# Kernel tuning notes

Measured on AMD Instinct MI355X. Metric: run time of the kernel, lower is better.

## Reference

```python
import jax, jax.numpy as jnp
import numpy as np

B, S, HID, H = 4, 2048, 768, 12
HD = HID // H  # head dim = 64
EPS = 1e-12


def _linear(x, w, b):
    # x: [B,S,HID], w: [HID,OUT] (already transposed to in x out), b: [OUT]
    return jnp.einsum('bsi,io->bso', x, w) + b


def _heads(x):
    # [B,S,HID] -> [B,H,S,HD]
    return x.reshape(B, S, H, HD).transpose(0, 2, 1, 3)


def _layernorm(x, g, b):
    mu = jnp.mean(x, axis=-1, keepdims=True)
    var = jnp.mean(jnp.square(x - mu), axis=-1, keepdims=True)
    return (x - mu) * jax.lax.rsqrt(var + EPS) * g + b


def _attend(q, k, v, mask):
    # q:[B,H,Sq,HD] k,v:[B,H,Sk,HD] mask:[B,1,1,Sk] additive
    scores = jnp.einsum('bhqd,bhkd->bhqk', q, k) / np.float32(np.sqrt(HD)) + mask
    probs = jax.nn.softmax(scores, axis=-1)  # dropout is identity in eval
    ctx = jnp.einsum('bhqk,bhkd->bhqd', probs, v)
    return ctx.transpose(0, 2, 1, 3).reshape(B, S, HID)


def setup_inputs() -> dict:
    key = jax.random.key(0)
    ks = jax.random.split(key, 20)
    std = 0.02
    mkw = lambda k: (jax.random.normal(k, (HID, HID), jnp.float32) * std)
    inp = {
        'input_tensor1': jax.random.normal(ks[0], (B, S, HID), jnp.float32),
        'attention_mask1': jnp.zeros((B, 1, 1, S), jnp.float32),
        'input_tensor2': jax.random.normal(ks[1], (B, S, HID), jnp.float32),
        'attention_mask2': jnp.zeros((B, 1, 1, S), jnp.float32),
        'q1_w': mkw(ks[2]), 'q1_b': jnp.zeros(HID),
        'k1_w': mkw(ks[3]), 'k1_b': jnp.zeros(HID),
        'v1_w': mkw(ks[4]), 'v1_b': jnp.zeros(HID),
        'q2_w': mkw(ks[5]), 'q2_b': jnp.zeros(HID),
        'k2_w': mkw(ks[6]), 'k2_b': jnp.zeros(HID),
        'v2_w': mkw(ks[7]), 'v2_b': jnp.zeros(HID),
        'd1_w': mkw(ks[8]), 'd1_b': jnp.zeros(HID),
        'd2_w': mkw(ks[9]), 'd2_b': jnp.zeros(HID),
        'ln1_g': jnp.ones(HID), 'ln1_b': jnp.zeros(HID),
        'ln2_g': jnp.ones(HID), 'ln2_b': jnp.zeros(HID),
    }
    return inp


def reference(input_tensor1, attention_mask1, input_tensor2, attention_mask2,
              q1_w, q1_b, k1_w, k1_b, v1_w, v1_b,
              q2_w, q2_b, k2_w, k2_b, v2_w, v2_b,
              d1_w, d1_b, d2_w, d2_b, ln1_g, ln1_b, ln2_g, ln2_b):
    q1 = _heads(_linear(input_tensor1, q1_w, q1_b))
    k1 = _heads(_linear(input_tensor1, k1_w, k1_b))
    v1 = _heads(_linear(input_tensor1, v1_w, v1_b))
    q2 = _heads(_linear(input_tensor2, q2_w, q2_b))
    k2 = _heads(_linear(input_tensor2, k2_w, k2_b))
    v2 = _heads(_linear(input_tensor2, v2_w, v2_b))
    # stream1 context: queries from stream2 attend keys/values of stream1
    ctx1 = _attend(q2, k1, v1, attention_mask1)
    # stream2 context: queries from stream1 attend keys/values of stream2
    ctx2 = _attend(q1, k2, v2, attention_mask2)
    h1 = _layernorm(_linear(ctx1, d1_w, d1_b) + input_tensor1, ln1_g, ln1_b)
    h2 = _layernorm(_linear(ctx2, d2_w, d2_b) + input_tensor2, ln2_g, ln2_b)
    return (h1, h2)
```

## Files before the change

### kernel.cpp

```cpp
#include <hip/hip_runtime.h>
#include <hip/hip_bf16.h>

#define BB   4
#define SS   2048
#define HID_ 768
#define NH   12
#define HD_  64
#define MR   8192
#define XELEMS 6291456

typedef __attribute__((ext_vector_type(8))) short short8;
typedef __attribute__((ext_vector_type(4))) float floatx4;

__device__ __forceinline__ unsigned short f2bf(float f) {
  union { float f; unsigned int u; } x; x.f = f;
  unsigned int r = x.u + 0x7fffu + ((x.u >> 16) & 1u);
  return (unsigned short)(r >> 16);
}

__device__ __forceinline__ unsigned short f2bf_fast(float f) {
  return (unsigned short)((__builtin_bit_cast(unsigned int, f) + 0x8000u) >> 16);
}

template <int CTRL>
__device__ __forceinline__ float dpp_ror(float x) {
  return __builtin_bit_cast(float, __builtin_amdgcn_update_dpp(
      0, __builtin_bit_cast(int, x), CTRL, 0xF, 0xF, true));
}
__device__ __forceinline__ float rowsum16(float x) {
  x += dpp_ror<0x128>(x);
  x += dpp_ror<0x124>(x);
  x += dpp_ror<0x122>(x);
  x += dpp_ror<0x121>(x);
  return x;
}

__device__ __forceinline__ void gload_lds16(const unsigned short* g, unsigned short* l) {
  __builtin_amdgcn_global_load_lds(
      (const __attribute__((address_space(1))) unsigned int*)g,
      (__attribute__((address_space(3))) unsigned int*)l, 16, 0, 0);
}

__global__ __launch_bounds__(256)
void cast_kernel(const float* __restrict__ src, unsigned short* __restrict__ dst, int n) {
  int i = (blockIdx.x * 256 + threadIdx.x) * 4;
  if (i < n) {
    float4 v = *(const float4*)(src + i);
    ushort4 o;
    o.x = f2bf(v.x); o.y = f2bf(v.y); o.z = f2bf(v.z); o.w = f2bf(v.w);
    *(ushort4*)(dst + i) = o;
  }
}

struct WArgs { const float* src[8]; unsigned short* dst[8]; };

__global__ __launch_bounds__(256)
void wcast_kernel(WArgs args) {
  __shared__ float tile[32][33];
  const int w = blockIdx.z;
  const float* __restrict__ src = args.src[w];
  unsigned short* __restrict__ dst = args.dst[w];
  const int n0 = blockIdx.x * 32, k0 = blockIdx.y * 32;
  const int tx = threadIdx.x & 31, ty = threadIdx.x >> 5;
  #pragma unroll
  for (int i = 0; i < 4; ++i)
    tile[ty + 8 * i][tx] = src[(size_t)(k0 + ty + 8 * i) * HID_ + n0 + tx];
  __syncthreads();
  #pragma unroll
  for (int i = 0; i < 4; ++i)
    dst[(size_t)(n0 + ty + 8 * i) * HID_ + k0 + tx] = f2bf(tile[tx][ty + 8 * i]);
}

struct GemmArgs {
  const unsigned short* A[6];
  const unsigned short* Bt[6];
  const float* bias[6];
  const float* resid[6];
  unsigned short* outb[6];
  float* outf[6];
  int tmode[6];
};

template <int MODE>
__global__ __launch_bounds__(256)
void gemm_kernel(GemmArgs args) {
  const int z = blockIdx.z;
  const unsigned short* __restrict__ A  = args.A[z];
  const unsigned short* __restrict__ Bt = args.Bt[z];
  const int m0 = blockIdx.x * 128;
  const int n0 = blockIdx.y * 128;

  __shared__ __align__(16) unsigned short a_sh[128 * 32];
  __shared__ __align__(16) unsigned short b_sh[128 * 32];

  const int tid  = threadIdx.x;
  const int lane = tid & 63;
  const int wave = tid >> 6;
  const int wm = (wave & 1) * 64;
  const int wn = (wave >> 1) * 64;
  const int l15 = lane & 15;
  const int ko  = lane >> 4;

  floatx4 acc[4][4];
  #pragma unroll
  for (int mt = 0; mt < 4; ++mt)
    #pragma unroll
    for (int nt = 0; nt < 4; ++nt) {
      floatx4 zz = {0.f, 0.f, 0.f, 0.f};
      acc[mt][nt] = zz;
    }

  const int ch0 = wave * 2;
  size_t aoff[2], boff[2];
  unsigned short *adst[2], *bdst[2];
  #pragma unroll
  for (int j = 0; j < 2; ++j) {
    const int ch = ch0 + j;
    const int row = ch * 16 + (lane >> 2);
    const int col = (lane & 3) * 8;
    aoff[j] = (size_t)(m0 + row) * 768 + col;
    boff[j] = (size_t)(n0 + row) * 768 + col;
    adst[j] = a_sh + ch * 512 + lane * 8;
    bdst[j] = b_sh + ch * 512 + lane * 8;
  }

  for (int k0 = 0; k0 < 768; k0 += 32) {
    #pragma unroll
    for (int j = 0; j < 2; ++j) {
      gload_lds16(A  + aoff[j] + k0, adst[j]);
      gload_lds16(Bt + boff[j] + k0, bdst[j]);
    }
    __syncthreads();
    short8 af[4], bfr[4];
    #pragma unroll
    for (int t = 0; t < 4; ++t) {
      af[t]  = *(const short8*)(a_sh + (wm + t * 16 + l15) * 32 + ko * 8);
      bfr[t] = *(const short8*)(b_sh + (wn + t * 16 + l15) * 32 + ko * 8);
    }
    #pragma unroll
    for (int mt = 0; mt < 4; ++mt)
      #pragma unroll
      for (int nt = 0; nt < 4; ++nt)
        acc[mt][nt] = __builtin_amdgcn_mfma_f32_16x16x32_bf16(af[mt], bfr[nt], acc[mt][nt], 0, 0, 0);
    __syncthreads();
  }

  if (MODE == 0) {
    const float* __restrict__ bias = args.bias[z];
    unsigned short* __restrict__ out = args.outb[z];
    if (args.tmode[z] == 0) {
      #pragma unroll
      for (int mt = 0; mt < 4; ++mt) {
        const int gm = m0 + wm + mt * 16 + ko * 4;
        #pragma unroll
        for (int nt = 0; nt < 4; ++nt) {
          const int gn = n0 + wn + nt * 16 + l15;
          const float bv = bias[gn];
          #pragma unroll
          for (int r = 0; r < 4; ++r)
            out[(size_t)(gm + r) * 768 + gn] = f2bf(acc[mt][nt][r] + bv);
        }
      }
    } else {
      #pragma unroll
      for (int mt = 0; mt < 4; ++mt) {
        const int gm = m0 + wm + mt * 16 + ko * 4;
        const int bb_ = gm >> 11;
        const int s   = gm & 2047;
        #pragma unroll
        for (int nt = 0; nt < 4; ++nt) {
          const int gn = n0 + wn + nt * 16 + l15;
          const float bv = bias[gn];
          const int h = gn >> 6, d = gn & 63;
          ushort4 o4;
          o4.x = f2bf(acc[mt][nt][0] + bv);
          o4.y = f2bf(acc[mt][nt][1] + bv);
          o4.z = f2bf(acc[mt][nt][2] + bv);
          o4.w = f2bf(acc[mt][nt][3] + bv);
          *(ushort4*)(out + ((size_t)((bb_ * 12 + h) * 64 + d)) * 2048 + s) = o4;
        }
      }
    }
  } else {
    const float* __restrict__ bias  = args.bias[z];
    const float* __restrict__ resid = args.resid[z];
    float* __restrict__ out = args.outf[z];
    #pragma unroll
    for (int mt = 0; mt < 4; ++mt) {
      const int gm = m0 + wm + mt * 16 + ko * 4;
      #pragma unroll
      for (int nt = 0; nt < 4; ++nt) {
        const int gn = n0 + wn + nt * 16 + l15;
        const float bv = bias[gn];
        #pragma unroll
        for (int r = 0; r < 4; ++r)
          out[(size_t)(gm + r) * 768 + gn] = acc[mt][nt][r] + bv + resid[(size_t)(gm + r) * 768 + gn];
      }
    }
  }
}

struct AttnArgs {
  const unsigned short* q[2];
  const unsigned short* k[2];
  const unsigned short* vt[2];
  const float* mask[2];
  unsigned short* ctx[2];
};

__global__ __launch_bounds__(256)
void attn_kernel(AttnArgs args) {
  const int z = blockIdx.z;
  const int b = z >> 1, w = z & 1;
  const int h = blockIdx.y;
  const int q0 = blockIdx.x * 64;

  const unsigned short* __restrict__ Q  = args.q[1 - w];
  const unsigned short* __restrict__ K  = args.k[w];
  const unsigned short* __restrict__ Vt = args.vt[w] + ((size_t)(b * 12 + h)) * 64 * 2048;
  const float* __restrict__ mask = args.mask[w] + (size_t)b * SS;
  unsigned short* __restrict__ O = args.ctx[w];

  __shared__ __align__(16) unsigned short k_sh[64 * 72];
  __shared__ __align__(16) unsigned short vT_sh[64 * 72];
  __shared__ __align__(16) unsigned short p_sh[4][16 * 72];

  const int tid  = threadIdx.x;
  const int lane = tid & 63;
  const int wave = tid >> 6;
  const int l15 = lane & 15;
  const int lq  = lane >> 4;

  const size_t qrow = (size_t)(b * SS + q0 + wave * 16 + l15) * 768 + h * 64;
  short8 qf[2];
  qf[0] = *(const short8*)(Q + qrow + lq * 8);
  qf[1] = *(const short8*)(Q + qrow + 32 + lq * 8);

  floatx4 oacc[4];
  #pragma unroll
  for (int nt = 0; nt < 4; ++nt) { floatx4 zz = {0.f,0.f,0.f,0.f}; oacc[nt] = zz; }
  float l_run[4] = {0.f, 0.f, 0.f, 0.f};

  const float SCL2 = 0.125f * 1.4426950408889634f;

  for (int kt = 0; kt < SS; kt += 64) {
    #pragma unroll
    for (int i = 0; i < 2; ++i) {
      const int c = tid * 2 + i;
      const int row = c >> 3;
      const int cb  = (c & 7) * 8;
      uint4 kv4 = *(const uint4*)(K + (size_t)(b * SS + kt + row) * 768 + h * 64 + cb);
      *(uint4*)(k_sh + row * 72 + cb) = kv4;
      uint4 vv4 = *(const uint4*)(Vt + (size_t)row * 2048 + kt + cb);
      *(uint4*)(vT_sh + row * 72 + cb) = vv4;
    }
    __syncthreads();

    floatx4 sacc[4];
    #pragma unroll
    for (int nt = 0; nt < 4; ++nt) {
      floatx4 zz = {0.f,0.f,0.f,0.f};
      sacc[nt] = zz;
      #pragma unroll
      for (int ks = 0; ks < 2; ++ks) {
        short8 bfr = *(const short8*)(k_sh + (nt * 16 + l15) * 72 + ks * 32 + lq * 8);
        sacc[nt] = __builtin_amdgcn_mfma_f32_16x16x32_bf16(qf[ks], bfr, sacc[nt], 0, 0, 0);
      }
    }

    float p[4][4], lad[4] = {0.f, 0.f, 0.f, 0.f};
    #pragma unroll
    for (int nt = 0; nt < 4; ++nt) {
      const float mk2 = mask[kt + nt * 16 + l15] * 1.4426950408889634f;
      #pragma unroll
      for (int r = 0; r < 4; ++r) {
        p[nt][r] = __builtin_amdgcn_exp2f(sacc[nt][r] * SCL2 + mk2);
        lad[r] += p[nt][r];
      }
    }
    #pragma unroll
    for (int r = 0; r < 4; ++r) l_run[r] += rowsum16(lad[r]);

    unsigned short* pw = p_sh[wave];
    #pragma unroll
    for (int nt = 0; nt < 4; ++nt)
      #pragma unroll
      for (int r = 0; r < 4; ++r)
        pw[(lq * 4 + r) * 72 + nt * 16 + l15] = f2bf_fast(p[nt][r]);

    #pragma unroll
    for (int nt = 0; nt < 4; ++nt) {
      #pragma unroll
      for (int ks = 0; ks < 2; ++ks) {
        short8 pf = *(const short8*)(pw + l15 * 72 + ks * 32 + lq * 8);
        short8 vf = *(const short8*)(vT_sh + (nt * 16 + l15) * 72 + ks * 32 + lq * 8);
        oacc[nt] = __builtin_amdgcn_mfma_f32_16x16x32_bf16(pf, vf, oacc[nt], 0, 0, 0);
      }
    }
    __syncthreads();
  }

  float inv[4];
  #pragma unroll
  for (int r = 0; r < 4; ++r) inv[r] = 1.f / l_run[r];
  #pragma unroll
  for (int nt = 0; nt < 4; ++nt) {
    #pragma unroll
    for (int r = 0; r < 4; ++r) {
      const int gq = q0 + wave * 16 + lq * 4 + r;
      const int gd = h * 64 + nt * 16 + l15;
      O[(size_t)(b * SS + gq) * 768 + gd] = f2bf(oacc[nt][r] * inv[r]);
    }
  }
}

__global__ __launch_bounds__(256)
void ln_kernel(const float* __restrict__ src, const float* __restrict__ g,
               const float* __restrict__ bta, float* __restrict__ out) {
  const int row = blockIdx.x;
  const int tid = threadIdx.x;
  const float* x = src + (size_t)row * 768;
  const float v0 = x[tid], v1 = x[tid + 256], v2 = x[tid + 512];
  float sum = v0 + v1 + v2;
  float sq  = v0 * v0 + v1 * v1 + v2 * v2;
  #pragma unroll
  for (int d = 1; d < 64; d <<= 1) {
    sum += __shfl_xor(sum, d, 64);
    sq  += __shfl_xor(sq, d, 64);
  }
  __shared__ float ssum[4], ssq[4];
  const int wave = tid >> 6, lane = tid & 63;
  if (lane == 0) { ssum[wave] = sum; ssq[wave] = sq; }
  __syncthreads();
  sum = ssum[0] + ssum[1] + ssum[2] + ssum[3];
  sq  = ssq[0] + ssq[1] + ssq[2] + ssq[3];
  const float mean = sum * (1.f / 768.f);
  const float var  = sq * (1.f / 768.f) - mean * mean;
  const float rs   = rsqrtf(var + 1e-12f);
  float* o = out + (size_t)row * 768;
  o[tid]       = (v0 - mean) * rs * g[tid]       + bta[tid];
  o[tid + 256] = (v1 - mean) * rs * g[tid + 256] + bta[tid + 256];
  o[tid + 512] = (v2 - mean) * rs * g[tid + 512] + bta[tid + 512];
}

extern "C" void kernel_launch(void* const* d_in, const int* in_sizes, int n_in,
                              void* d_out, int out_size, void* d_ws, size_t ws_size,
                              hipStream_t stream) {
  const float* x1    = (const float*)d_in[0];
  const float* mask1 = (const float*)d_in[1];
  const float* x2    = (const float*)d_in[2];
  const float* mask2 = (const float*)d_in[3];

  char* ws = (char*)d_ws;
  const size_t SZ_X = (size_t)MR * HID_ * 2;
  const size_t SZ_W = (size_t)HID_ * HID_ * 2;

  unsigned short* xb0 = (unsigned short*)(ws);
  unsigned short* xb1 = (unsigned short*)(ws + SZ_X);
  unsigned short* wtb[8];
  for (int i = 0; i < 8; ++i) wtb[i] = (unsigned short*)(ws + 2 * SZ_X + i * SZ_W);
  char* qbase = ws + 2 * SZ_X + 8 * SZ_W;
  unsigned short* qkvb[6];
  for (int i = 0; i < 6; ++i) qkvb[i] = (unsigned short*)(qbase + i * SZ_X);
  unsigned short* ctxb[2];
  ctxb[0] = (unsigned short*)(qbase + 6 * SZ_X);
  ctxb[1] = (unsigned short*)(qbase + 7 * SZ_X);
  float* projb[2];
  projb[0] = (float*)(qbase);
  projb[1] = (float*)(qbase + 2 * SZ_X);

  cast_kernel<<<XELEMS / 1024, 256, 0, stream>>>(x1, xb0, XELEMS);
  cast_kernel<<<XELEMS / 1024, 256, 0, stream>>>(x2, xb1, XELEMS);

  WArgs wa;
  for (int z = 0; z < 8; ++z) { wa.src[z] = (const float*)d_in[4 + 2 * z]; wa.dst[z] = wtb[z]; }
  wcast_kernel<<<dim3(24, 24, 8), 256, 0, stream>>>(wa);

  GemmArgs ga = {};
  for (int z = 0; z < 6; ++z) {
    ga.A[z]    = (z < 3) ? xb0 : xb1;
    ga.Bt[z]   = wtb[z];
    ga.bias[z] = (const float*)d_in[5 + 2 * z];
    ga.outb[z] = qkvb[z];
    ga.tmode[z] = (z == 2 || z == 5) ? 2 : 0;
  }
  gemm_kernel<0><<<dim3(64, 6, 6), 256, 0, stream>>>(ga);

  AttnArgs aa;
  aa.q[0] = qkvb[0]; aa.q[1] = qkvb[3];
  aa.k[0] = qkvb[1]; aa.k[1] = qkvb[4];
  aa.vt[0] = qkvb[2]; aa.vt[1] = qkvb[5];
  aa.mask[0] = mask1; aa.mask[1] = mask2;
  aa.ctx[0] = ctxb[0]; aa.ctx[1] = ctxb[1];
  attn_kernel<<<dim3(32, 12, 8), 256, 0, stream>>>(aa);

  GemmArgs gp = {};
  for (int w = 0; w < 2; ++w) {
    gp.A[w]     = ctxb[w];
    gp.Bt[w]    = wtb[6 + w];
    gp.bias[w]  = (const float*)d_in[17 + 2 * w];
    gp.resid[w] = (w == 0) ? x1 : x2;
    gp.outf[w]  = projb[w];
  }
  gemm_kernel<1><<<dim3(64, 6, 2), 256, 0, stream>>>(gp);

  float* out = (float*)d_out;
  ln_kernel<<<MR, 256, 0, stream>>>(projb[0], (const float*)d_in[20], (const float*)d_in[21], out);
  ln_kernel<<<MR, 256, 0, stream>>>(projb[1], (const float*)d_in[22], (const float*)d_in[23], out + XELEMS);
}
```

Baseline: 525.4 us.

## Double-buffer K/V via direct global-to-LDS loads and double query rows per block

The attention kernel now processes 128 queries per block (two 16-row tiles per wave), halving the grid and reusing each K/V tile across twice as many queries. K and V tiles are loaded with direct global-to-LDS loads into a double-buffered, XOR-swizzled shared buffer, and the next tile is prefetched while the current one is computed, with explicit vmcnt waits and raw barriers. The aim is to hide global load latency and cut redundant K/V traffic. In exchange, register pressure rises (the launch bounds now ask for 3 blocks per CU), and the kernel depends on a gload_lds16 helper and a hand-counted waitcnt.

```diff
diff --git a/kernel.cpp b/kernel.cpp
--- a/kernel.cpp
+++ b/kernel.cpp
@@ -208,12 +208,12 @@
   unsigned short* ctx[2];
 };
 
-__global__ __launch_bounds__(256)
+__global__ __launch_bounds__(256, 3)
 void attn_kernel(AttnArgs args) {
   const int z = blockIdx.z;
   const int b = z >> 1, w = z & 1;
   const int h = blockIdx.y;
-  const int q0 = blockIdx.x * 64;
+  const int q0 = blockIdx.x * 128;
 
   const unsigned short* __restrict__ Q  = args.q[1 - w];
   const unsigned short* __restrict__ K  = args.k[w];
@@ -221,95 +221,164 @@
   const float* __restrict__ mask = args.mask[w] + (size_t)b * SS;
   unsigned short* __restrict__ O = args.ctx[w];
 
-  __shared__ __align__(16) unsigned short k_sh[64 * 72];
-  __shared__ __align__(16) unsigned short vT_sh[64 * 72];
-  __shared__ __align__(16) unsigned short p_sh[4][16 * 72];
+  __shared__ __align__(16) unsigned short kv_sh[2][8192];
+  __shared__ __align__(16) unsigned short p_sh[4][32 * 72];
 
   const int tid  = threadIdx.x;
   const int lane = tid & 63;
   const int wave = tid >> 6;
   const int l15 = lane & 15;
   const int lq  = lane >> 4;
-
-  const size_t qrow = (size_t)(b * SS + q0 + wave * 16 + l15) * 768 + h * 64;
-  short8 qf[2];
-  qf[0] = *(const short8*)(Q + qrow + lq * 8);
-  qf[1] = *(const short8*)(Q + qrow + 32 + lq * 8);
-
-  floatx4 oacc[4];
-  #pragma unroll
-  for (int nt = 0; nt < 4; ++nt) { floatx4 zz = {0.f,0.f,0.f,0.f}; oacc[nt] = zz; }
-  float l_run[4] = {0.f, 0.f, 0.f, 0.f};
+  const int sw8 = (lq ^ (l15 & 3)) * 8;
+
+  const unsigned short* gsrc[4];
+  int gadv[4];
+  #pragma unroll
+  for (int j = 0; j < 4; ++j) {
+    const int c  = wave * 4 + j;
+    const int rl = lane >> 2;
+    const int jb = (lane & 3) ^ (rl & 3);
+    if (c < 8) {
+      const int ks  = (c >> 2) & 1;
+      const int row = (c & 3) * 16 + rl;
+      gsrc[j] = K + (size_t)(b * SS + row) * 768 + h * 64 + ks * 32 + jb * 8;
+      gadv[j] = 64 * 768;
+    } else {
+      const int c2 = c - 8;
+      const int ks = (c2 >> 2) & 1;
+      const int dr = (c2 & 3) * 16 + rl;
+      gsrc[j] = Vt + (size_t)dr * 2048 + ks * 32 + jb * 8;
+      gadv[j] = 64;
+    }
+  }
+
+  short8 qf[2][2];
+  #pragma unroll
+  for (int mt = 0; mt < 2; ++mt) {
+    const size_t qrow = (size_t)(b * SS + q0 + wave * 32 + mt * 16 + l15) * 768 + h * 64;
+    qf[mt][0] = *(const short8*)(Q + qrow + lq * 8);
+    qf[mt][1] = *(const short8*)(Q + qrow + 32 + lq * 8);
+  }
+
+  floatx4 oacc[2][4];
+  #pragma unroll
+  for (int mt = 0; mt < 2; ++mt)
+    #pragma unroll
+    for (int nt = 0; nt < 4; ++nt) { floatx4 zz = {0.f,0.f,0.f,0.f}; oacc[mt][nt] = zz; }
+  float l_run[2][4] = {{0.f,0.f,0.f,0.f},{0.f,0.f,0.f,0.f}};
 
   const float SCL2 = 0.125f * 1.4426950408889634f;
-
-  for (int kt = 0; kt < SS; kt += 64) {
-    #pragma unroll
-    for (int i = 0; i < 2; ++i) {
-      const int c = tid * 2 + i;
-      const int row = c >> 3;
-      const int cb  = (c & 7) * 8;
-      uint4 kv4 = *(const uint4*)(K + (size_t)(b * SS + kt + row) * 768 + h * 64 + cb);
-      *(uint4*)(k_sh + row * 72 + cb) = kv4;
-      uint4 vv4 = *(const uint4*)(Vt + (size_t)row * 2048 + kt + cb);
-      *(uint4*)(vT_sh + row * 72 + cb) = vv4;
-    }
-    __syncthreads();
-
-    floatx4 sacc[4];
+  const float L2E  = 1.4426950408889634f;
+
+  float mk_cur[4], mk_nxt[4];
+  #pragma unroll
+  for (int nt = 0; nt < 4; ++nt) mk_cur[nt] = mask[nt * 16 + l15];
+  #pragma unroll
+  for (int j = 0; j < 4; ++j) {
+    gload_lds16(gsrc[j], &kv_sh[0][0] + (wave * 4 + j) * 512);
+    gsrc[j] += gadv[j];
+  }
+
+  unsigned short* const pw = p_sh[wave];
+  const int NT = SS / 64;
+
+  for (int t = 0; t < NT; ++t) {
+    const int cb = t & 1;
+    if (t + 1 < NT) {
+      const int kt1 = (t + 1) * 64;
+      #pragma unroll
+      for (int nt = 0; nt < 4; ++nt) mk_nxt[nt] = mask[kt1 + nt * 16 + l15];
+      #pragma unroll
+      for (int j = 0; j < 4; ++j) {
+        gload_lds16(gsrc[j], &kv_sh[cb ^ 1][0] + (wave * 4 + j) * 512);
+        gsrc[j] += gadv[j];
+      }
+      asm volatile("s_waitcnt vmcnt(8)" ::: "memory");
+    } else {
+      asm volatile("s_waitcnt vmcnt(0)" ::: "memory");
+    }
+    __builtin_amdgcn_s_barrier();
+    asm volatile("" ::: "memory");
+
+    const unsigned short* kb = &kv_sh[cb][0];
+    const unsigned short* vb = &kv_sh[cb][4096];
+
+    short8 kf[4][2];
     #pragma unroll
     for (int nt = 0; nt < 4; ++nt) {
-      floatx4 zz = {0.f,0.f,0.f,0.f};
-      sacc[nt] = zz;
-      #pragma unroll
-      for (int ks = 0; ks < 2; ++ks) {
-        short8 bfr = *(const short8*)(k_sh + (nt * 16 + l15) * 72 + ks * 32 + lq * 8);
-        sacc[nt] = __builtin_amdgcn_mfma_f32_16x16x32_bf16(qf[ks], bfr, sacc[nt], 0, 0, 0);
-      }
-    }
-
-    float p[4][4], lad[4] = {0.f, 0.f, 0.f, 0.f};
+      const int ro = (nt * 16 + l15) * 32 + sw8;
+      kf[nt][0] = *(const short8*)(kb + ro);
+      kf[nt][1] = *(const short8*)(kb + 2048 + ro);
+    }
+    floatx4 sacc[2][4];
+    #pragma unroll
+    for (int mt = 0; mt < 2; ++mt)
+      #pragma unroll
+      for (int nt = 0; nt < 4; ++nt) {
+        floatx4 zz = {0.f,0.f,0.f,0.f};
+        sacc[mt][nt] = __builtin_amdgcn_mfma_f32_16x16x32_bf16(qf[mt][0], kf[nt][0], zz, 0, 0, 0);
+        sacc[mt][nt] = __builtin_amdgcn_mfma_f32_16x16x32_bf16(qf[mt][1], kf[nt][1], sacc[mt][nt], 0, 0, 0);
+      }
+
+    #pragma unroll
+    for (int mt = 0; mt < 2; ++mt) {
+      float lad[4] = {0.f, 0.f, 0.f, 0.f};
+      #pragma unroll
+      for (int nt = 0; nt < 4; ++nt) {
+        const float mk2 = mk_cur[nt] * L2E;
+        #pragma unroll
+        for (int r = 0; r < 4; ++r) {
+          const float p = __builtin_amdgcn_exp2f(sacc[mt][nt][r] * SCL2 + mk2);
+          lad[r] += p;
+          pw[(mt * 16 + lq * 4 + r) * 72 + nt * 16 + l15] = f2bf_fast(p);
+        }
+      }
+      #pragma unroll
+      for (int r = 0; r < 4; ++r) l_run[mt][r] += rowsum16(lad[r]);
+    }
+
+    short8 vf[4][2];
     #pragma unroll
     for (int nt = 0; nt < 4; ++nt) {
-      const float mk2 = mask[kt + nt * 16 + l15] * 1.4426950408889634f;
+      const int ro = (nt * 16 + l15) * 32 + sw8;
+      vf[nt][0] = *(const short8*)(vb + ro);
+      vf[nt][1] = *(const short8*)(vb + 2048 + ro);
+    }
+    short8 pf[2][2];
+    #pragma unroll
+    for (int mt = 0; mt < 2; ++mt) {
+      pf[mt][0] = *(const short8*)(pw + (mt * 16 + l15) * 72 + lq * 8);
+      pf[mt][1] = *(const short8*)(pw + (mt * 16 + l15) * 72 + 32 + lq * 8);
+    }
+    #pragma unroll
+    for (int mt = 0; mt < 2; ++mt)
+      #pragma unroll
+      for (int nt = 0; nt < 4; ++nt) {
+        oacc[mt][nt] = __builtin_amdgcn_mfma_f32_16x16x32_bf16(pf[mt][0], vf[nt][0], oacc[mt][nt], 0, 0, 0);
+        oacc[mt][nt] = __builtin_amdgcn_mfma_f32_16x16x32_bf16(pf[mt][1], vf[nt][1], oacc[mt][nt], 0, 0, 0);
+      }
+
+    asm volatile("" ::: "memory");
+    __builtin_amdgcn_s_barrier();
+    asm volatile("" ::: "memory");
+
+    #pragma unroll
+    for (int nt = 0; nt < 4; ++nt) mk_cur[nt] = mk_nxt[nt];
+  }
+
+  #pragma unroll
+  for (int mt = 0; mt < 2; ++mt) {
+    float inv[4];
+    #pragma unroll
+    for (int r = 0; r < 4; ++r) inv[r] = 1.f / l_run[mt][r];
+    #pragma unroll
+    for (int nt = 0; nt < 4; ++nt) {
       #pragma unroll
       for (int r = 0; r < 4; ++r) {
-        p[nt][r] = __builtin_amdgcn_exp2f(sacc[nt][r] * SCL2 + mk2);
-        lad[r] += p[nt][r];
-      }
-    }
-    #pragma unroll
-    for (int r = 0; r < 4; ++r) l_run[r] += rowsum16(lad[r]);
-
-    unsigned short* pw = p_sh[wave];
-    #pragma unroll
-    for (int nt = 0; nt < 4; ++nt)
-      #pragma unroll
-      for (int r = 0; r < 4; ++r)
-        pw[(lq * 4 + r) * 72 + nt * 16 + l15] = f2bf_fast(p[nt][r]);
-
-    #pragma unroll
-    for (int nt = 0; nt < 4; ++nt) {
-      #pragma unroll
-      for (int ks = 0; ks < 2; ++ks) {
-        short8 pf = *(const short8*)(pw + l15 * 72 + ks * 32 + lq * 8);
-        short8 vf = *(const short8*)(vT_sh + (nt * 16 + l15) * 72 + ks * 32 + lq * 8);
-        oacc[nt] = __builtin_amdgcn_mfma_f32_16x16x32_bf16(pf, vf, oacc[nt], 0, 0, 0);
-      }
-    }
-    __syncthreads();
-  }
-
-  float inv[4];
-  #pragma unroll
-  for (int r = 0; r < 4; ++r) inv[r] = 1.f / l_run[r];
-  #pragma unroll
-  for (int nt = 0; nt < 4; ++nt) {
-    #pragma unroll
-    for (int r = 0; r < 4; ++r) {
-      const int gq = q0 + wave * 16 + lq * 4 + r;
-      const int gd = h * 64 + nt * 16 + l15;
-      O[(size_t)(b * SS + gq) * 768 + gd] = f2bf(oacc[nt][r] * inv[r]);
+        const int gq = q0 + wave * 32 + mt * 16 + lq * 4 + r;
+        const int gd = h * 64 + nt * 16 + l15;
+        O[(size_t)(b * SS + gq) * 768 + gd] = f2bf(oacc[mt][nt][r] * inv[r]);
+      }
     }
   }
 }
@@ -392,7 +461,7 @@
   aa.vt[0] = qkvb[2]; aa.vt[1] = qkvb[5];
   aa.mask[0] = mask1; aa.mask[1] = mask2;
   aa.ctx[0] = ctxb[0]; aa.ctx[1] = ctxb[1];
-  attn_kernel<<<dim3(32, 12, 8), 256, 0, stream>>>(aa);
+  attn_kernel<<<dim3(16, 12, 8), 256, 0, stream>>>(aa);
 
   GemmArgs gp = {};
   for (int w = 0; w < 2; ++w) {
```

After: 487.0 us. 7.3% less time.
